# Optimization experiments

Measured on AMD Instinct MI355X. Metric: run time of the kernel, lower is better.

The kernel has to match this reference:

```python
import jax, jax.numpy as jnp
import numpy as np

B, S, D, H = 2, 2048, 2048, 16
HD = D // H          # 128, even for RoPE
GS = 0.1             # governance_strength
ROPE_BASE = 10000.0


def _rope_cos_sin(seq_len, dtype):
    # inv_freq over pairs of dims: [HD/2]
    inv_freq = 1.0 / (ROPE_BASE ** (jnp.arange(0, HD, 2, dtype=jnp.float32) / HD))
    t = jnp.arange(seq_len, dtype=jnp.float32)
    freqs = jnp.outer(t, inv_freq)          # [S, HD/2]
    return jnp.cos(freqs).astype(dtype), jnp.sin(freqs).astype(dtype)


def _apply_rope(x, cos, sin):
    # x: [B,H,S,HD]; cos/sin: [S,HD/2] -> broadcast over batch/heads
    x1, x2 = jnp.split(x, 2, axis=-1)
    c = cos[None, None, :, :]
    s = sin[None, None, :, :]
    return jnp.concatenate([x1 * c - x2 * s, x2 * c + x1 * s], axis=-1)


def setup_inputs() -> dict:
    key = jax.random.key(0)
    ks = jax.random.split(key, 8)
    sc = 1.0 / np.sqrt(D)
    return {
        "x": jax.random.normal(ks[0], (B, S, D), jnp.float32),
        "Wq": jax.random.normal(ks[1], (D, D), jnp.float32) * sc,
        "Wk": jax.random.normal(ks[2], (D, D), jnp.float32) * sc,
        "Wv": jax.random.normal(ks[3], (D, D), jnp.float32) * sc,
        "Wo": jax.random.normal(ks[4], (D, D), jnp.float32) * sc,
        "bo": jnp.zeros((D,), jnp.float32),
        "policy_mask": jax.random.uniform(ks[5], (1, H, S, S), jnp.float32),
        "memory_weights": jax.random.uniform(ks[6], (B, 1, 1, S), jnp.float32),
    }


def reference(x, Wq, Wk, Wv, Wo, bo, policy_mask, memory_weights):
    dtype = x.dtype
    scale = HD ** -0.5

    def heads(t):
        return t.reshape(B, S, H, HD).transpose(0, 2, 1, 3)  # [B,H,S,HD]

    q = heads(x @ Wq)
    k = heads(x @ Wk)
    v = heads(x @ Wv)

    cos, sin = _rope_cos_sin(S, dtype)
    q = _apply_rope(q, cos, sin)
    k = _apply_rope(k, cos, sin)

    scores = jnp.einsum("bhqd,bhkd->bhqk", q, k) * scale  # [B,H,S,S]

    # governance bias: policy term + memory-aware log term
    bias = policy_mask * GS + jnp.log1p(memory_weights * GS + 1e-8)
    scores = scores + bias

    # causal mask (no KV cache: kv_len == q_len)
    causal = jnp.tril(jnp.ones((S, S), bool))[None, None]
    scores = jnp.where(causal, scores, jnp.asarray(-1e9, dtype))

    attn = jax.nn.softmax(scores, axis=-1)
    out = jnp.einsum("bhqk,bhkd->bhqd", attn, v)          # [B,H,S,HD]
    out = out.transpose(0, 2, 1, 3).reshape(B, S, D)
    return out @ Wo + bo
```

## Files before the change

kernel.cpp:

```cpp
#include <hip/hip_runtime.h>
#include <hip/hip_bf16.h>
#include <math.h>

#define B_ 2
#define S_ 2048
#define D_ 2048
#define H_ 16
#define HD_ 128
#define NT_ (B_*S_)
#define GS_ 0.1f

typedef _Float16 half8 __attribute__((__vector_size__(16)));
typedef _Float16 half4v __attribute__((__vector_size__(8)));
typedef float f32x4 __attribute__((__vector_size__(16)));

#define VMCNT(n) asm volatile("s_waitcnt vmcnt(" #n ")" ::: "memory")

__device__ __forceinline__ void gload_lds16(const void* g, void* s) {
  __builtin_amdgcn_global_load_lds(
      (const __attribute__((address_space(1))) unsigned int*)g,
      (__attribute__((address_space(3))) unsigned int*)s, 16, 0, 0);
}


__global__ void cvt_f32_to_f16(const float* __restrict__ in, _Float16* __restrict__ out, int n4) {
  int i = blockIdx.x * blockDim.x + threadIdx.x;
  if (i >= n4) return;
  float4 v = ((const float4*)in)[i];
  half4v o = { (_Float16)v.x, (_Float16)v.y, (_Float16)v.z, (_Float16)v.w };
  ((half4v*)out)[i] = o;
}

__global__ void transpose_to_f16(const float* __restrict__ in, _Float16* __restrict__ out, int R, int C) {
  __shared__ float t[32][33];
  int c0 = blockIdx.x*32, r0 = blockIdx.y*32;
  int tx = threadIdx.x, ty = threadIdx.y;
#pragma unroll
  for (int j = 0; j < 32; j += 8)
    t[ty+j][tx] = in[(size_t)(r0+ty+j)*C + c0+tx];
  __syncthreads();
#pragma unroll
  for (int j = 0; j < 32; j += 8)
    out[(size_t)(c0+ty+j)*R + r0+tx] = (_Float16)t[tx][ty+j];
}

__global__ void prep_tables(const float* __restrict__ mw, float* __restrict__ cost,
                            float* __restrict__ sint, float* __restrict__ lmw) {
  int t = blockIdx.x*256 + threadIdx.x;
  if (t < S_*64) {
    int s = t >> 6, d = t & 63;
    float inv = (float)pow(10000.0, -(double)(2*d)/(double)HD_);
    float f = (float)s * inv;
    cost[t] = cosf(f);
    sint[t] = sinf(f);
  }
  if (t < B_*S_) lmw[t] = log1pf(mw[t]*GS_ + 1e-8f);
}


#define QUAD(MH,NH) do{ \
  _Pragma("unroll") for (int dmi=0;dmi<2;++dmi) \
  _Pragma("unroll") for (int dni=0;dni<2;++dni) \
  _Pragma("unroll") for (int kk=0;kk<2;++kk) \
    acc[(MH)*2+dmi][(NH)*2+dni] = __builtin_amdgcn_mfma_f32_16x16x32_f16( \
        a[dmi][kk], b[(NH)*2+dni][kk], acc[(MH)*2+dmi][(NH)*2+dni],0,0,0); \
}while(0)

template<bool F32OUT>
__global__ __launch_bounds__(512) void gemm256(
    const _Float16* __restrict__ A, const _Float16* __restrict__ Bt,
    void* __restrict__ Cout, const float* __restrict__ bias,
    int M, int N, int K)
{
  __shared__ __align__(16) char Ar[4][16384];
  __shared__ __align__(16) char Br[4][16384];
  int nwg = gridDim.x*gridDim.y;
  int bid = blockIdx.y*gridDim.x + blockIdx.x;
  int swz = ((nwg&7)==0) ? ((bid&7)*(nwg>>3) + (bid>>3)) : bid;
  int bx = swz % gridDim.x, by = swz / gridDim.x;
  int n0 = bx*128, m0 = by*256;
  int tid = threadIdx.x;
  int w = tid>>6, l = tid&63, lhi = l>>4, llo = l&15;
  int wr = w>>1, wc = w&1;
  int nkt = K>>6;

  auto stage = [&](char* dst, const _Float16* src){
#pragma unroll
    for (int i=0;i<2;++i){
      int s = i*512 + tid;
      int row = s>>3, ch = (s&7)^(row&7);
      gload_lds16(src + (size_t)row*K + ch*8, dst + i*8192 + w*1024);
    }
  };
  auto stageA = [&](int h, int tt){ stage(Ar[(2*tt+h)&3], A + (size_t)(m0+h*128)*K + (size_t)tt*64); };
  auto stageB = [&](int tt){ stage(Br[tt&3], Bt + (size_t)n0*K + (size_t)tt*64); };

  const f32x4 fz = {0.f,0.f,0.f,0.f};
  f32x4 acc[4][4];
#pragma unroll
  for (int i=0;i<4;++i)
#pragma unroll
    for (int j=0;j<4;++j) acc[i][j] = fz;

  stageB(0); stageA(0,0); stageA(1,0);
  if (nkt > 1) { stageB(1); stageA(0,1); VMCNT(4); }
  else         { VMCNT(0); }
  __builtin_amdgcn_sched_barrier(0);
  __builtin_amdgcn_s_barrier();

  int hA = wr>>1;
  int rb = (wr&1)*64;

  for (int t = 0; t < nkt; ++t) {
    const char* Au = Ar[(2*t+hA)&3];
    const char* Bu = Br[t&3];
    half8 a[2][2], b[4][2];
#pragma unroll
    for (int dmi=0;dmi<2;++dmi){
      int rr = rb + dmi*16 + llo;
#pragma unroll
      for (int kk=0;kk<2;++kk)
        a[dmi][kk] = *(const half8*)(Au + rr*128 + (((kk*4+lhi)^(rr&7))<<4));
    }
#pragma unroll
    for (int ni=0;ni<4;++ni){
      int rn = wc*64 + ni*16 + llo;
#pragma unroll
      for (int kk=0;kk<2;++kk)
        b[ni][kk] = *(const half8*)(Bu + rn*128 + (((kk*4+lhi)^(rn&7))<<4));
    }
    if (t+1 < nkt) stageA(1, t+1);
    __builtin_amdgcn_s_barrier();
    __builtin_amdgcn_s_setprio(1);
    QUAD(0,0);
    __builtin_amdgcn_s_setprio(0);
    __builtin_amdgcn_s_barrier();
    if (t+2 < nkt) stageB(t+2);
    __builtin_amdgcn_s_setprio(1);
    QUAD(0,1);
    __builtin_amdgcn_s_setprio(0);
    __builtin_amdgcn_s_barrier();
#pragma unroll
    for (int dmi=0;dmi<2;++dmi){
      int rr = rb + 32 + dmi*16 + llo;
#pragma unroll
      for (int kk=0;kk<2;++kk)
        a[dmi][kk] = *(const half8*)(Au + rr*128 + (((kk*4+lhi)^(rr&7))<<4));
    }
    __builtin_amdgcn_s_setprio(1);
    QUAD(1,0);
    __builtin_amdgcn_s_setprio(0);
    __builtin_amdgcn_s_barrier();
    if (t+2 < nkt) stageA(0, t+2);
    __builtin_amdgcn_s_setprio(1);
    QUAD(1,1);
    __builtin_amdgcn_s_setprio(0);
    if (t+2 < nkt) { VMCNT(4); } else { VMCNT(0); }
    __builtin_amdgcn_sched_barrier(0);
    __builtin_amdgcn_s_barrier();
  }

#pragma unroll
  for (int mi=0;mi<4;++mi)
#pragma unroll
    for (int ni=0;ni<4;++ni)
#pragma unroll
      for (int r=0;r<4;++r){
        int row = m0 + wr*64 + mi*16 + lhi*4 + r;
        int col = n0 + wc*64 + ni*16 + llo;
        if constexpr (F32OUT)
          ((float*)Cout)[(size_t)row*N + col] = acc[mi][ni][r] + bias[col];
        else
          ((_Float16*)Cout)[(size_t)row*N + col] = (_Float16)acc[mi][ni][r];
      }
}

__global__ void rope_qk(const _Float16* __restrict__ qkv, const float* __restrict__ cost,
                        const float* __restrict__ sint, _Float16* __restrict__ Qr,
                        _Float16* __restrict__ Kr) {
  int token = blockIdx.x;
  int b = token >> 11, s = token & (S_-1);
  int t = threadIdx.x;
  int isk = t >> 7, u = t & 127;
  int hh = u >> 3, dd0 = (u & 7)*8;
  const _Float16* src = qkv + (size_t)token*(3*D_) + (size_t)isk*D_ + hh*128;
  half8 a  = *(const half8*)(src + dd0);
  half8 bb = *(const half8*)(src + 64 + dd0);
  half8 lo, hi;
#pragma unroll
  for (int j = 0; j < 8; ++j) {
    float c  = cost[s*64 + dd0 + j];
    float sn = sint[s*64 + dd0 + j];
    float x1 = (float)a[j], x2 = (float)bb[j];
    lo[j] = (_Float16)(x1*c - x2*sn);
    hi[j] = (_Float16)(x2*c + x1*sn);
  }
  _Float16* dst = (isk ? Kr : Qr) + ((size_t)(b*H_ + hh)*S_ + s)*HD_;
  *(half8*)(dst + dd0) = lo;
  *(half8*)(dst + 64 + dd0) = hi;
}

__global__ void v_transpose(const _Float16* __restrict__ qkv, _Float16* __restrict__ Vt) {
  __shared__ _Float16 tile[64][33];
  int st = blockIdx.x*64;
  int dt = blockIdx.y*32;
  int bh = blockIdx.z;
  int b = bh >> 4, h = bh & 15;
  int t = threadIdx.x;
  int s = t >> 2, dc = (t & 3)*8;
  half8 v = *(const half8*)(qkv + (size_t)(b*S_ + st + s)*(3*D_) + 2*D_ + h*128 + dt + dc);
#pragma unroll
  for (int j = 0; j < 8; ++j) tile[s][dc+j] = v[j];
  __syncthreads();
  int d = t >> 3, sc = (t & 7)*8;
  half8 o;
#pragma unroll
  for (int j = 0; j < 8; ++j) o[j] = tile[sc+j][d];
  *(half8*)(Vt + ((size_t)bh*HD_ + dt + d)*S_ + st + sc) = o;
}

__global__ __launch_bounds__(256) void attn_kernel(
    const _Float16* __restrict__ Qr, const _Float16* __restrict__ Kr,
    const _Float16* __restrict__ Vt, const float* __restrict__ policy,
    const float* __restrict__ lmw, _Float16* __restrict__ Ob)
{
  __shared__ __align__(16) _Float16 Kl[64*128];
  __shared__ __align__(16) _Float16 Vl[128*64];
  __shared__ __align__(16) _Float16 Pl[4][16*64];
  int bx = blockIdx.x;
  int qt = (S_/64) - 1 - (bx / (B_*H_));
  int rem = bx % (B_*H_);
  int h = rem >> 1;
  int b = rem & 1;
  int bh = b*H_ + h;
  const _Float16* Qb = Qr + (size_t)bh*S_*HD_;
  const _Float16* Kb = Kr + (size_t)bh*S_*HD_;
  const _Float16* Vb = Vt + (size_t)bh*HD_*S_;
  const float* pol = policy + (size_t)h*S_*S_;
  int tid = threadIdx.x;
  int w = tid >> 6, l = tid & 63;
  int lhi = l >> 4, llo = l & 15;
  int q0 = qt*64 + w*16;

  half8 qf[4];
#pragma unroll
  for (int c = 0; c < 4; ++c)
    qf[c] = *(const half8*)(Qb + (size_t)(q0+llo)*HD_ + c*32 + lhi*8);

  const f32x4 fz = {0.f,0.f,0.f,0.f};
  f32x4 outacc[8];
#pragma unroll
  for (int i = 0; i < 8; ++i) outacc[i] = fz;
  float m_[4], l_[4];
#pragma unroll
  for (int r = 0; r < 4; ++r) { m_[r] = -INFINITY; l_[r] = 0.f; }

  const float scale = 0.08838834764831845f;
  _Float16* Pw = &Pl[w][0];

  for (int t = 0; t <= qt; ++t) {
    int kv0 = t*64;
#pragma unroll
    for (int i = 0; i < 4; ++i) {
      int sid = i*256 + tid;
      int key = sid >> 4;
      int ck = (sid & 15) ^ (key & 7);
      gload_lds16(Kb + (size_t)(kv0+key)*HD_ + ck*8, (char*)Kl + (size_t)(i*256 + w*64)*16);
      int dv = sid >> 3;
      int cv = (sid & 7) ^ (dv & 7);
      gload_lds16(Vb + (size_t)dv*S_ + kv0 + cv*8, (char*)Vl + (size_t)(i*256 + w*64)*16);
    }
    __syncthreads();

    f32x4 sacc[4];
#pragma unroll
    for (int kf = 0; kf < 4; ++kf) sacc[kf] = fz;
    __builtin_amdgcn_s_setprio(1);
#pragma unroll
    for (int kf = 0; kf < 4; ++kf) {
      int key = kf*16 + llo;
#pragma unroll
      for (int c = 0; c < 4; ++c) {
        int ch = (c*4 + lhi) ^ (key & 7);
        half8 kfr = *(const half8*)((const char*)Kl + key*256 + ch*16);
        sacc[kf] = __builtin_amdgcn_mfma_f32_16x16x32_f16(qf[c], kfr, sacc[kf], 0, 0, 0);
      }
    }
    __builtin_amdgcn_s_setprio(0);

    bool diag = (t == qt);
    float lm[4];
#pragma unroll
    for (int kf = 0; kf < 4; ++kf) lm[kf] = lmw[b*S_ + kv0 + kf*16 + llo];
    float pv[4][4];
#pragma unroll
    for (int kf = 0; kf < 4; ++kf) {
      int gk = kv0 + kf*16 + llo;
#pragma unroll
      for (int r = 0; r < 4; ++r) {
        int gq = q0 + lhi*4 + r;
        float v = sacc[kf][r]*scale + pol[(size_t)gq*S_ + gk]*GS_ + lm[kf];
        if (diag && gk > gq) v = -1e9f;
        pv[kf][r] = v;
      }
    }
    float fct[4];
#pragma unroll
    for (int r = 0; r < 4; ++r) {
      float mx = fmaxf(fmaxf(pv[0][r], pv[1][r]), fmaxf(pv[2][r], pv[3][r]));
#pragma unroll
      for (int s = 8; s > 0; s >>= 1) mx = fmaxf(mx, __shfl_xor(mx, s, 16));
      float mnew = fmaxf(m_[r], mx);
      fct[r] = __expf(m_[r] - mnew);
      m_[r] = mnew;
    }
    float rsum[4] = {0.f,0.f,0.f,0.f};
#pragma unroll
    for (int kf = 0; kf < 4; ++kf)
#pragma unroll
      for (int r = 0; r < 4; ++r) {
        float p = __expf(pv[kf][r] - m_[r]);
        pv[kf][r] = p;
        rsum[r] += p;
      }
#pragma unroll
    for (int r = 0; r < 4; ++r) {
      float rs = rsum[r];
#pragma unroll
      for (int s = 8; s > 0; s >>= 1) rs += __shfl_xor(rs, s, 16);
      l_[r] = l_[r]*fct[r] + rs;
    }
#pragma unroll
    for (int i = 0; i < 8; ++i) {
      f32x4 o = outacc[i];
      o[0] *= fct[0]; o[1] *= fct[1]; o[2] *= fct[2]; o[3] *= fct[3];
      outacc[i] = o;
    }
#pragma unroll
    for (int kf = 0; kf < 4; ++kf)
#pragma unroll
      for (int r = 0; r < 4; ++r) {
        int pq = lhi*4 + r, pk = kf*16 + llo;
        int byte = (pq*128 + pk*2) ^ ((pq & 7) << 4);
        *(_Float16*)((char*)Pw + byte) = (_Float16)pv[kf][r];
      }
    __builtin_amdgcn_s_setprio(1);
#pragma unroll
    for (int kc = 0; kc < 2; ++kc) {
      int ch = (kc*4 + lhi) ^ (llo & 7);
      half8 pa = *(const half8*)((const char*)Pw + llo*128 + ch*16);
#pragma unroll
      for (int db = 0; db < 8; ++db) {
        int d = db*16 + llo;
        int chv = (kc*4 + lhi) ^ (d & 7);
        half8 vb = *(const half8*)((const char*)Vl + d*128 + chv*16);
        outacc[db] = __builtin_amdgcn_mfma_f32_16x16x32_f16(pa, vb, outacc[db], 0, 0, 0);
      }
    }
    __builtin_amdgcn_s_setprio(0);
    __syncthreads();
  }
#pragma unroll
  for (int db = 0; db < 8; ++db)
#pragma unroll
    for (int r = 0; r < 4; ++r) {
      int gq = q0 + lhi*4 + r;
      float o = outacc[db][r] / l_[r];
      Ob[((size_t)b*S_ + gq)*D_ + h*HD_ + db*16 + llo] = (_Float16)o;
    }
}


extern "C" void kernel_launch(void* const* d_in, const int* in_sizes, int n_in,
                              void* d_out, int out_size, void* d_ws, size_t ws_size,
                              hipStream_t stream) {
  const float* x   = (const float*)d_in[0];
  const float* Wq  = (const float*)d_in[1];
  const float* Wk  = (const float*)d_in[2];
  const float* Wv  = (const float*)d_in[3];
  const float* Wo  = (const float*)d_in[4];
  const float* bo  = (const float*)d_in[5];
  const float* pol = (const float*)d_in[6];
  const float* mw  = (const float*)d_in[7];
  float* out = (float*)d_out;

  char* p = (char*)d_ws;
  auto take = [&](size_t bytes) { char* r = p; p += (bytes + 255) & ~(size_t)255; return r; };
  _Float16* xb   = (_Float16*)take((size_t)NT_*D_*2);
  _Float16* Wt   = (_Float16*)take((size_t)3*D_*D_*2);
  _Float16* Wot  = (_Float16*)take((size_t)D_*D_*2);
  _Float16* qkv  = (_Float16*)take((size_t)NT_*3*D_*2);
  _Float16* Qr   = (_Float16*)take((size_t)B_*H_*S_*HD_*2);
  _Float16* Kr   = (_Float16*)take((size_t)B_*H_*S_*HD_*2);
  _Float16* Vtb  = (_Float16*)take((size_t)B_*H_*S_*HD_*2);
  _Float16* Ob   = (_Float16*)take((size_t)NT_*D_*2);
  float* cost = (float*)take((size_t)S_*64*4);
  float* sint = (float*)take((size_t)S_*64*4);
  float* lmwb = (float*)take((size_t)B_*S_*4);

  cvt_f32_to_f16<<<(NT_*D_/4 + 255)/256, 256, 0, stream>>>(x, xb, NT_*D_/4);
  transpose_to_f16<<<dim3(64,64), dim3(32,8), 0, stream>>>(Wq, Wt,                    D_, D_);
  transpose_to_f16<<<dim3(64,64), dim3(32,8), 0, stream>>>(Wk, Wt +   (size_t)D_*D_,  D_, D_);
  transpose_to_f16<<<dim3(64,64), dim3(32,8), 0, stream>>>(Wv, Wt + 2*(size_t)D_*D_,  D_, D_);
  transpose_to_f16<<<dim3(64,64), dim3(32,8), 0, stream>>>(Wo, Wot, D_, D_);
  prep_tables<<<512, 256, 0, stream>>>(mw, cost, sint, lmwb);

  gemm256<false><<<dim3(3*D_/128, NT_/256), 512, 0, stream>>>(xb, Wt, qkv, nullptr, NT_, 3*D_, D_);
  rope_qk<<<NT_, 256, 0, stream>>>(qkv, cost, sint, Qr, Kr);
  v_transpose<<<dim3(S_/64, HD_/32, B_*H_), 256, 0, stream>>>(qkv, Vtb);
  attn_kernel<<<B_*H_*(S_/64), 256, 0, stream>>>(Qr, Kr, Vtb, pol, lmwb, Ob);
  gemm256<true><<<dim3(D_/128, NT_/256), 512, 0, stream>>>(Ob, Wot, out, bo, NT_, D_, D_);
}
```

Baseline: 373.5 us.

## Restructure GEMM LDS pipeline to triple-buffered full k-tile prefetch

Switches the GEMM's shared-memory ring from 4 A-half/4 B buffers to 6 A-half/3 B buffers. Each iteration now issues the whole next-next k-tile (B plus both A halves) at once and merges the four MFMA quads into two groups with fewer barriers. The aim is a deeper, simpler prefetch pipeline and less barrier overhead, at the cost of 144KB of LDS instead of 128KB and coarser interleaving of loads with MFMA work.

```diff
diff --git a/kernel.cpp b/kernel.cpp
--- a/kernel.cpp
+++ b/kernel.cpp
@@ -67,13 +67,13 @@
 }while(0)
 
 template<bool F32OUT>
-__global__ __launch_bounds__(512) void gemm256(
+__global__ __launch_bounds__(512) void gemmA(
     const _Float16* __restrict__ A, const _Float16* __restrict__ Bt,
     void* __restrict__ Cout, const float* __restrict__ bias,
     int M, int N, int K)
 {
-  __shared__ __align__(16) char Ar[4][16384];
-  __shared__ __align__(16) char Br[4][16384];
+  __shared__ __align__(16) char Ar[6][16384];
+  __shared__ __align__(16) char Br[3][16384];
   int nwg = gridDim.x*gridDim.y;
   int bid = blockIdx.y*gridDim.x + blockIdx.x;
   int swz = ((nwg&7)==0) ? ((bid&7)*(nwg>>3) + (bid>>3)) : bid;
@@ -92,8 +92,12 @@
       gload_lds16(src + (size_t)row*K + ch*8, dst + i*8192 + w*1024);
     }
   };
-  auto stageA = [&](int h, int tt){ stage(Ar[(2*tt+h)&3], A + (size_t)(m0+h*128)*K + (size_t)tt*64); };
-  auto stageB = [&](int tt){ stage(Br[tt&3], Bt + (size_t)n0*K + (size_t)tt*64); };
+  auto stageA = [&](int tt){
+    const _Float16* base = A + (size_t)m0*K + (size_t)tt*64;
+    stage(Ar[(2*tt)%6],   base);
+    stage(Ar[(2*tt+1)%6], base + (size_t)128*K);
+  };
+  auto stageB = [&](int tt){ stage(Br[tt%3], Bt + (size_t)n0*K + (size_t)tt*64); };
 
   const f32x4 fz = {0.f,0.f,0.f,0.f};
   f32x4 acc[4][4];
@@ -102,9 +106,8 @@
 #pragma unroll
     for (int j=0;j<4;++j) acc[i][j] = fz;
 
-  stageB(0); stageA(0,0); stageA(1,0);
-  if (nkt > 1) { stageB(1); stageA(0,1); VMCNT(4); }
-  else         { VMCNT(0); }
+  stageA(0); stageB(0); stageA(1); stageB(1);
+  VMCNT(6);
   __builtin_amdgcn_sched_barrier(0);
   __builtin_amdgcn_s_barrier();
 
@@ -112,8 +115,8 @@
   int rb = (wr&1)*64;
 
   for (int t = 0; t < nkt; ++t) {
-    const char* Au = Ar[(2*t+hA)&3];
-    const char* Bu = Br[t&3];
+    const char* Au = Ar[(2*t+hA)%6];
+    const char* Bu = Br[t%3];
     half8 a[2][2], b[4][2];
 #pragma unroll
     for (int dmi=0;dmi<2;++dmi){
@@ -129,16 +132,13 @@
       for (int kk=0;kk<2;++kk)
         b[ni][kk] = *(const half8*)(Bu + rn*128 + (((kk*4+lhi)^(rn&7))<<4));
     }
-    if (t+1 < nkt) stageA(1, t+1);
+    if (t+2 < nkt) { stageB(t+2); stageA(t+2); }
+    __builtin_amdgcn_sched_barrier(0);
     __builtin_amdgcn_s_barrier();
     __builtin_amdgcn_s_setprio(1);
-    QUAD(0,0);
+    QUAD(0,0); QUAD(0,1);
     __builtin_amdgcn_s_setprio(0);
-    __builtin_amdgcn_s_barrier();
-    if (t+2 < nkt) stageB(t+2);
-    __builtin_amdgcn_s_setprio(1);
-    QUAD(0,1);
-    __builtin_amdgcn_s_setprio(0);
+    __builtin_amdgcn_sched_barrier(0);
     __builtin_amdgcn_s_barrier();
 #pragma unroll
     for (int dmi=0;dmi<2;++dmi){
@@ -147,15 +147,12 @@
       for (int kk=0;kk<2;++kk)
         a[dmi][kk] = *(const half8*)(Au + rr*128 + (((kk*4+lhi)^(rr&7))<<4));
     }
+    __builtin_amdgcn_sched_barrier(0);
+    __builtin_amdgcn_s_barrier();
     __builtin_amdgcn_s_setprio(1);
-    QUAD(1,0);
+    QUAD(1,0); QUAD(1,1);
     __builtin_amdgcn_s_setprio(0);
-    __builtin_amdgcn_s_barrier();
-    if (t+2 < nkt) stageA(0, t+2);
-    __builtin_amdgcn_s_setprio(1);
-    QUAD(1,1);
-    __builtin_amdgcn_s_setprio(0);
-    if (t+2 < nkt) { VMCNT(4); } else { VMCNT(0); }
+    if (t+2 < nkt) { VMCNT(6); } else { VMCNT(0); }
     __builtin_amdgcn_sched_barrier(0);
     __builtin_amdgcn_s_barrier();
   }
@@ -405,9 +402,9 @@
   transpose_to_f16<<<dim3(64,64), dim3(32,8), 0, stream>>>(Wo, Wot, D_, D_);
   prep_tables<<<512, 256, 0, stream>>>(mw, cost, sint, lmwb);
 
-  gemm256<false><<<dim3(3*D_/128, NT_/256), 512, 0, stream>>>(xb, Wt, qkv, nullptr, NT_, 3*D_, D_);
+  gemmA<false><<<dim3(3*D_/128, NT_/256), 512, 0, stream>>>(xb, Wt, qkv, nullptr, NT_, 3*D_, D_);
   rope_qk<<<NT_, 256, 0, stream>>>(qkv, cost, sint, Qr, Kr);
   v_transpose<<<dim3(S_/64, HD_/32, B_*H_), 256, 0, stream>>>(qkv, Vtb);
   attn_kernel<<<B_*H_*(S_/64), 256, 0, stream>>>(Qr, Kr, Vtb, pol, lmwb, Ob);
-  gemm256<true><<<dim3(D_/128, NT_/256), 512, 0, stream>>>(Ob, Wot, out, bo, NT_, D_, D_);
-}
+  gemmA<true><<<dim3(D_/128, NT_/256), 512, 0, stream>>>(Ob, Wot, out, bo, NT_, D_, D_);
+}
```

Result: no change. 372.1 us (-0.4%).
